# Kernel tuning notes

Hardware: AMD Instinct MI355X
Metric: run time of the kernel (lower is better)

## Reference

```python
import jax, jax.numpy as jnp
import numpy as np

HIDDEN = 2048
INTER = 768
N_EXPERTS = 16
TOP_K = 2
B, S = 4, 2048


def setup_inputs() -> dict:
    key = jax.random.key(0)
    ks = jax.random.split(key, 5)
    scale = 0.02
    return {
        "hidden_states": jax.random.normal(ks[0], (B, S, HIDDEN), dtype=jnp.float32),
        # nn.Linear weight layout: [out_features, in_features]
        "gate_w": jax.random.normal(ks[1], (N_EXPERTS, HIDDEN), dtype=jnp.float32) * scale,
        "w_gate": jax.random.normal(ks[2], (N_EXPERTS, INTER, HIDDEN), dtype=jnp.float32) * scale,
        "w_up": jax.random.normal(ks[3], (N_EXPERTS, INTER, HIDDEN), dtype=jnp.float32) * scale,
        "w_down": jax.random.normal(ks[4], (N_EXPERTS, HIDDEN, INTER), dtype=jnp.float32) * scale,
    }


def _moe_forward(hidden_states, gate_w, w_gate, w_up, w_down):
    b, s, h = hidden_states.shape
    x = hidden_states.reshape(-1, h)                      # [T, H]
    t = x.shape[0]
    logits = x @ gate_w.T                                 # [T, E]
    probs = jax.nn.softmax(logits, axis=-1)
    top_vals, top_idx = jax.lax.top_k(probs, TOP_K)       # [T, K]
    top_vals = top_vals / jnp.sum(top_vals, axis=-1, keepdims=True)
    # combine weights per token per expert (zero if not routed)
    comb = jnp.zeros((t, N_EXPERTS), dtype=x.dtype)
    comb = comb.at[jnp.arange(t)[:, None], top_idx].add(top_vals)  # [T, E]

    out = jnp.zeros_like(x)
    for e in range(N_EXPERTS):  # small fixed loop over experts
        g = x @ w_gate[e].T                               # [T, I]
        u = x @ w_up[e].T                                 # [T, I]
        y = (jax.nn.silu(g) * u) @ w_down[e].T            # [T, H]
        out = out + comb[:, e:e + 1] * y
    return out.reshape(b, s, h)


def reference(hidden_states, gate_w, w_gate, w_up, w_down):
    return _moe_forward(hidden_states, gate_w, w_gate, w_up, w_down)
```

## Files before the change

kernel.cpp:

```cpp
#include <hip/hip_runtime.h>
#include <hip/hip_bf16.h>

#define NTOK 8192
#define HID 2048
#define INTER 768
#define NEXP 16

typedef __bf16 bf16x8 __attribute__((ext_vector_type(8)));
typedef float f32x4 __attribute__((ext_vector_type(4)));

typedef const __attribute__((address_space(1))) void gvoid_t;
typedef __attribute__((address_space(3))) void lvoid_t;

static __device__ __forceinline__ void load_lds16(const void* g, void* l) {
  __builtin_amdgcn_global_load_lds((gvoid_t*)g, (lvoid_t*)l, 16, 0, 0);
}

static __device__ __forceinline__ unsigned short f2bf(float f) {
  unsigned int u = __float_as_uint(f);
  u += 0x7FFFu + ((u >> 16) & 1u);
  return (unsigned short)(u >> 16);
}

static __device__ __forceinline__ float bf2f(unsigned short b) {
  return __uint_as_float(((unsigned int)b) << 16);
}

#define SYNC_PIPE                                     \
  asm volatile("s_waitcnt vmcnt(0)" ::: "memory");    \
  __builtin_amdgcn_s_barrier();

__global__ __launch_bounds__(256) void cvt3_kernel(
    const float* __restrict__ s0, const float* __restrict__ s1, const float* __restrict__ s2,
    unsigned short* __restrict__ dst0, unsigned short* __restrict__ dst1,
    unsigned short* __restrict__ dst2, int n) {
  const float* src = (blockIdx.y == 0) ? s0 : (blockIdx.y == 1) ? s1 : s2;
  unsigned short* dst = (blockIdx.y == 0) ? dst0 : (blockIdx.y == 1) ? dst1 : dst2;
  int i = (blockIdx.x * 256 + threadIdx.x) * 4;
  int stride = gridDim.x * 256 * 4;
  for (; i < n; i += stride) {
    float4 v = *reinterpret_cast<const float4*>(src + i);
    ushort4 o;
    o.x = f2bf(v.x); o.y = f2bf(v.y); o.z = f2bf(v.z); o.w = f2bf(v.w);
    *reinterpret_cast<ushort4*>(dst + i) = o;
  }
}

__global__ __launch_bounds__(256) void router_kernel(const float* __restrict__ x,
                                                     const float* __restrict__ gw,
                                                     int* __restrict__ te,
                                                     float* __restrict__ tw,
                                                     unsigned short* __restrict__ Xb) {
  const int lane = threadIdx.x & 63;
  const int wid = threadIdx.x >> 6;
  const int t0 = (blockIdx.x * 4 + wid) * 2;
  const float4* xa = reinterpret_cast<const float4*>(x + (size_t)t0 * HID);
  const float4* xb = xa + HID / 4;
  const float4* g4 = reinterpret_cast<const float4*>(gw);

  float4 va[8], vb[8];
#pragma unroll
  for (int j = 0; j < 8; ++j) {
    va[j] = xa[lane + 64 * j];
    vb[j] = xb[lane + 64 * j];
  }
  ushort4* oa = reinterpret_cast<ushort4*>(Xb + (size_t)t0 * HID);
  ushort4* ob = oa + HID / 4;
#pragma unroll
  for (int j = 0; j < 8; ++j) {
    ushort4 u;
    u.x = f2bf(va[j].x); u.y = f2bf(va[j].y); u.z = f2bf(va[j].z); u.w = f2bf(va[j].w);
    oa[lane + 64 * j] = u;
    u.x = f2bf(vb[j].x); u.y = f2bf(vb[j].y); u.z = f2bf(vb[j].z); u.w = f2bf(vb[j].w);
    ob[lane + 64 * j] = u;
  }

  float accA[NEXP], accB[NEXP];
#pragma unroll
  for (int e = 0; e < NEXP; ++e) { accA[e] = 0.f; accB[e] = 0.f; }
#pragma unroll
  for (int e = 0; e < NEXP; ++e) {
#pragma unroll
    for (int j = 0; j < 8; ++j) {
      float4 g = g4[e * (HID / 4) + lane + 64 * j];
      accA[e] += va[j].x * g.x + va[j].y * g.y + va[j].z * g.z + va[j].w * g.w;
      accB[e] += vb[j].x * g.x + vb[j].y * g.y + vb[j].z * g.z + vb[j].w * g.w;
    }
  }
#pragma unroll
  for (int e = 0; e < NEXP; ++e) {
#pragma unroll
    for (int m = 32; m >= 1; m >>= 1) {
      accA[e] += __shfl_xor(accA[e], m);
      accB[e] += __shfl_xor(accB[e], m);
    }
  }
  if (lane == 0) {
#pragma unroll
    for (int k = 0; k < 2; ++k) {
      const float* acc = k ? accB : accA;
      int t = t0 + k;
      float b0 = -1e30f; int i0 = 0;
#pragma unroll
      for (int e = 0; e < NEXP; ++e) { if (acc[e] > b0) { b0 = acc[e]; i0 = e; } }
      float b1 = -1e30f; int i1 = 0;
#pragma unroll
      for (int e = 0; e < NEXP; ++e) { if (e != i0 && acc[e] > b1) { b1 = acc[e]; i1 = e; } }
      float w0 = 1.f / (1.f + __expf(b1 - b0));
      te[2 * t] = i0; te[2 * t + 1] = i1;
      tw[2 * t] = w0; tw[2 * t + 1] = 1.f - w0;
    }
  }
}

__global__ __launch_bounds__(256) void build_kernel(
    const int* __restrict__ te, const float* __restrict__ tw,
    int* __restrict__ counts, int* __restrict__ offsets,
    int* __restrict__ tok_flat, float* __restrict__ w_flat,
    int* __restrict__ tok_slot,
    int* __restrict__ tile_map, int* __restrict__ n_tiles) {
  __shared__ int lds_cnt[NEXP][257];
  __shared__ int lds_off[NEXP];
  const int tid = threadIdx.x;
  const int lane = tid & 63;
  const int wv = tid >> 6;

  int cnt[NEXP];
#pragma unroll
  for (int ex = 0; ex < NEXP; ++ex) cnt[ex] = 0;
  for (int i = 0; i < 64; ++i) {
    int e = te[tid * 64 + i];
#pragma unroll
    for (int ex = 0; ex < NEXP; ++ex) cnt[ex] += (e == ex) ? 1 : 0;
  }
#pragma unroll
  for (int ex = 0; ex < NEXP; ++ex) lds_cnt[ex][tid] = cnt[ex];
  __syncthreads();

  for (int ex = wv * 4; ex < wv * 4 + 4; ++ex) {
    int carry = 0;
    for (int c = 0; c < 4; ++c) {
      int v = lds_cnt[ex][c * 64 + lane];
      int s = v;
#pragma unroll
      for (int d = 1; d < 64; d <<= 1) {
        int o = __shfl_up(s, d);
        if (lane >= d) s += o;
      }
      lds_cnt[ex][c * 64 + lane] = carry + s - v;
      carry += __shfl(s, 63);
    }
    if (lane == 0) lds_cnt[ex][256] = carry;
  }
  __syncthreads();

  if (tid == 0) {
    int run = 0, nt = 0;
    for (int e = 0; e < NEXP; ++e) {
      int tot = lds_cnt[e][256];
      counts[e] = tot;
      offsets[e] = run;
      lds_off[e] = run;
      for (int m0 = 0; m0 < tot; m0 += 128) tile_map[nt++] = (e << 16) | m0;
      run += tot;
    }
    *n_tiles = nt;
  }
  __syncthreads();

  int base[NEXP];
#pragma unroll
  for (int ex = 0; ex < NEXP; ++ex) base[ex] = lds_off[ex] + lds_cnt[ex][tid];
  for (int i = 0; i < 64; ++i) {
    int idx = tid * 64 + i;
    int e = te[idx];
    float w = tw[idx];
    int pos = 0;
#pragma unroll
    for (int ex = 0; ex < NEXP; ++ex) {
      if (e == ex) { pos = base[ex]; base[ex] = pos + 1; }
    }
    tok_flat[pos] = idx >> 1;
    w_flat[pos] = w;
    tok_slot[idx] = pos;
  }
}

__global__ __launch_bounds__(256, 3) void gemm_gu_kernel(
    const unsigned short* __restrict__ Xb,
    const unsigned short* __restrict__ Wg,
    const unsigned short* __restrict__ Wu,
    const int* __restrict__ counts, const int* __restrict__ offsets,
    const int* __restrict__ tok_flat,
    const int* __restrict__ tile_map, const int* __restrict__ n_tiles,
    unsigned short* __restrict__ Hf) {
  const int bid = blockIdx.x;
  const int cpx = gridDim.x >> 3;
  const int wg = (bid & 7) * cpx + (bid >> 3);
  const int y = wg / 12;
  if (y >= *n_tiles) return;
  const int xb = wg - y * 12;
  const int tm = tile_map[y];
  const int e = tm >> 16, m0 = tm & 0xFFFF;
  const int cnt = counts[e];
  const int off = offsets[e];
  const int n0 = xb * 64;

  __shared__ __align__(16) unsigned short As0[128 * 32], As1[128 * 32];
  __shared__ __align__(16) unsigned short Bg0[64 * 32], Bg1[64 * 32];
  __shared__ __align__(16) unsigned short Bu0[64 * 32], Bu1[64 * 32];

  const int tid = threadIdx.x;
  const int lane = tid & 63;
  const int wid = tid >> 6;
  const int rl = tid >> 2;
  const int srcc = ((tid & 3) ^ ((tid >> 3) & 3)) * 8;
  const int d0 = tid * 8;
  const int d1 = d0 + 64 * 32;

  const int r0 = m0 + rl, r1 = r0 + 64;
  const int s0 = (r0 < cnt) ? off + r0 : off;
  const int s1 = (r1 < cnt) ? off + r1 : off;
  const unsigned short* aptr0 = Xb + (size_t)tok_flat[s0] * HID + srcc;
  const unsigned short* aptr1 = Xb + (size_t)tok_flat[s1] * HID + srcc;
  const unsigned short* gptr0 = Wg + ((size_t)e * INTER + n0 + rl) * HID + srcc;
  const unsigned short* uptr0 = Wu + ((size_t)e * INTER + n0 + rl) * HID + srcc;

  f32x4 zero = {0.f, 0.f, 0.f, 0.f};
  f32x4 accG[4][2], accU[4][2];
#pragma unroll
  for (int i = 0; i < 4; ++i)
#pragma unroll
    for (int j = 0; j < 2; ++j) { accG[i][j] = zero; accU[i][j] = zero; }

  const int wm = (wid >> 1) * 64;
  const int wn = (wid & 1) * 32;
  const int fr = lane & 15;
  const int cs = (((lane >> 4) ^ ((lane >> 1) & 3)) * 8);

#define STAGE_GU(AS, BGS, BUS, kt)           \
  {                                          \
    load_lds16(aptr0 + (kt), (AS) + d0);     \
    load_lds16(aptr1 + (kt), (AS) + d1);     \
    load_lds16(gptr0 + (kt), (BGS) + d0);    \
    load_lds16(uptr0 + (kt), (BUS) + d0);    \
  }

#define COMPUTE_GU(AS, BGS, BUS)                                                       \
  {                                                                                    \
    bf16x8 af[4], bg[2], bu[2];                                                        \
    _Pragma("unroll") for (int i = 0; i < 4; ++i)                                      \
      af[i] = *reinterpret_cast<const bf16x8*>((AS) + (wm + i * 16 + fr) * 32 + cs);   \
    _Pragma("unroll") for (int j = 0; j < 2; ++j) {                                    \
      bg[j] = *reinterpret_cast<const bf16x8*>((BGS) + (wn + j * 16 + fr) * 32 + cs);  \
      bu[j] = *reinterpret_cast<const bf16x8*>((BUS) + (wn + j * 16 + fr) * 32 + cs);  \
    }                                                                                  \
    _Pragma("unroll") for (int i = 0; i < 4; ++i)                                      \
      _Pragma("unroll") for (int j = 0; j < 2; ++j) {                                  \
        accG[i][j] = __builtin_amdgcn_mfma_f32_16x16x32_bf16(af[i], bg[j], accG[i][j], 0, 0, 0); \
        accU[i][j] = __builtin_amdgcn_mfma_f32_16x16x32_bf16(af[i], bu[j], accU[i][j], 0, 0, 0); \
      }                                                                                \
  }

  STAGE_GU(As0, Bg0, Bu0, 0);
  SYNC_PIPE
#pragma unroll 1
  for (int kt = 0; kt < HID; kt += 64) {
    STAGE_GU(As1, Bg1, Bu1, kt + 32);
    COMPUTE_GU(As0, Bg0, Bu0);
    SYNC_PIPE
    if (kt + 64 < HID) STAGE_GU(As0, Bg0, Bu0, kt + 64);
    COMPUTE_GU(As1, Bg1, Bu1);
    SYNC_PIPE
  }
#undef STAGE_GU
#undef COMPUTE_GU

  const int lr = (lane >> 4) * 4;
  const int lc = lane & 15;
#pragma unroll
  for (int i = 0; i < 4; ++i) {
#pragma unroll
    for (int r = 0; r < 4; ++r) {
      int m = wm + i * 16 + lr + r;
      if (m0 + m < cnt) {
        size_t base = (size_t)(off + m0 + m) * INTER + (size_t)(n0 + wn + lc);
#pragma unroll
        for (int j = 0; j < 2; ++j) {
          float g = accG[i][j][r];
          float u = accU[i][j][r];
          float h = g / (1.f + __expf(-g)) * u;
          Hf[base + j * 16] = f2bf(h);
        }
      }
    }
  }
}

__global__ __launch_bounds__(256, 4) void gemm_y_kernel(
    const unsigned short* __restrict__ Hf,
    const unsigned short* __restrict__ Wd,
    const int* __restrict__ counts, const int* __restrict__ offsets,
    const float* __restrict__ w_flat,
    const int* __restrict__ tile_map, const int* __restrict__ n_tiles,
    unsigned short* __restrict__ Yf) {
  const int bid = blockIdx.x;
  const int cpx = gridDim.x >> 3;
  const int wg = (bid & 7) * cpx + (bid >> 3);
  const int y = wg / 32;
  if (y >= *n_tiles) return;
  const int xb = wg - y * 32;
  const int tm = tile_map[y];
  const int e = tm >> 16, m0 = tm & 0xFFFF;
  const int cnt = counts[e];
  const int off = offsets[e];
  const int n0 = xb * 64;

  __shared__ __align__(16) unsigned short As0[128 * 32], As1[128 * 32];
  __shared__ __align__(16) unsigned short Bs0[64 * 32], Bs1[64 * 32];

  const int tid = threadIdx.x;
  const int lane = tid & 63;
  const int wid = tid >> 6;
  const int rl = tid >> 2;
  const int srcc = ((tid & 3) ^ ((tid >> 3) & 3)) * 8;
  const int d0 = tid * 8;
  const int d1 = d0 + 64 * 32;

  const int r0 = m0 + rl, r1 = r0 + 64;
  const int s0 = (r0 < cnt) ? off + r0 : off;
  const int s1 = (r1 < cnt) ? off + r1 : off;
  const unsigned short* aptr0 = Hf + (size_t)s0 * INTER + srcc;
  const unsigned short* aptr1 = Hf + (size_t)s1 * INTER + srcc;
  const unsigned short* bptr0 = Wd + ((size_t)e * HID + n0 + rl) * INTER + srcc;

  f32x4 zero = {0.f, 0.f, 0.f, 0.f};
  f32x4 acc[4][2];
#pragma unroll
  for (int i = 0; i < 4; ++i)
#pragma unroll
    for (int j = 0; j < 2; ++j) acc[i][j] = zero;

  const int wm = (wid >> 1) * 64;
  const int wn = (wid & 1) * 32;
  const int fr = lane & 15;
  const int cs = (((lane >> 4) ^ ((lane >> 1) & 3)) * 8);

#define STAGE_Y(AS, BS, kt)               \
  {                                       \
    load_lds16(aptr0 + (kt), (AS) + d0);  \
    load_lds16(aptr1 + (kt), (AS) + d1);  \
    load_lds16(bptr0 + (kt), (BS) + d0);  \
  }

#define COMPUTE_Y(AS, BS)                                                              \
  {                                                                                    \
    bf16x8 af[4], bf_[2];                                                              \
    _Pragma("unroll") for (int i = 0; i < 4; ++i)                                      \
      af[i] = *reinterpret_cast<const bf16x8*>((AS) + (wm + i * 16 + fr) * 32 + cs);   \
    _Pragma("unroll") for (int j = 0; j < 2; ++j)                                      \
      bf_[j] = *reinterpret_cast<const bf16x8*>((BS) + (wn + j * 16 + fr) * 32 + cs);  \
    _Pragma("unroll") for (int i = 0; i < 4; ++i)                                      \
      _Pragma("unroll") for (int j = 0; j < 2; ++j)                                    \
        acc[i][j] = __builtin_amdgcn_mfma_f32_16x16x32_bf16(af[i], bf_[j], acc[i][j], 0, 0, 0); \
  }

  STAGE_Y(As0, Bs0, 0);
  SYNC_PIPE
#pragma unroll 1
  for (int kt = 0; kt < INTER; kt += 64) {
    STAGE_Y(As1, Bs1, kt + 32);
    COMPUTE_Y(As0, Bs0);
    SYNC_PIPE
    if (kt + 64 < INTER) STAGE_Y(As0, Bs0, kt + 64);
    COMPUTE_Y(As1, Bs1);
    SYNC_PIPE
  }
#undef STAGE_Y
#undef COMPUTE_Y

  const int lr = (lane >> 4) * 4;
  const int lc = lane & 15;
#pragma unroll
  for (int i = 0; i < 4; ++i) {
#pragma unroll
    for (int r = 0; r < 4; ++r) {
      int m = wm + i * 16 + lr + r;
      if (m0 + m < cnt) {
        int slot = off + m0 + m;
        float w = w_flat[slot];
        size_t base = (size_t)slot * HID + (size_t)(n0 + wn + lc);
#pragma unroll
        for (int j = 0; j < 2; ++j) Yf[base + j * 16] = f2bf(w * acc[i][j][r]);
      }
    }
  }
}

__global__ __launch_bounds__(256) void combine_kernel(const unsigned short* __restrict__ Yf,
                                                      const int* __restrict__ tok_slot,
                                                      float* __restrict__ out) {
  const int t = blockIdx.x;
  const int c = threadIdx.x * 8;
  const int s0 = tok_slot[2 * t];
  const int s1 = tok_slot[2 * t + 1];
  const ushort4* p0 = reinterpret_cast<const ushort4*>(Yf + (size_t)s0 * HID + c);
  const ushort4* p1 = reinterpret_cast<const ushort4*>(Yf + (size_t)s1 * HID + c);
  ushort4 a0 = p0[0], a1 = p0[1];
  ushort4 b0 = p1[0], b1 = p1[1];
  float4 o0, o1;
  o0.x = bf2f(a0.x) + bf2f(b0.x);
  o0.y = bf2f(a0.y) + bf2f(b0.y);
  o0.z = bf2f(a0.z) + bf2f(b0.z);
  o0.w = bf2f(a0.w) + bf2f(b0.w);
  o1.x = bf2f(a1.x) + bf2f(b1.x);
  o1.y = bf2f(a1.y) + bf2f(b1.y);
  o1.z = bf2f(a1.z) + bf2f(b1.z);
  o1.w = bf2f(a1.w) + bf2f(b1.w);
  float4* op = reinterpret_cast<float4*>(out + (size_t)t * HID + c);
  op[0] = o0;
  op[1] = o1;
}

extern "C" void kernel_launch(void* const* d_in, const int* in_sizes, int n_in,
                              void* d_out, int out_size, void* d_ws, size_t ws_size,
                              hipStream_t stream) {
  const float* x  = (const float*)d_in[0];
  const float* gw = (const float*)d_in[1];
  const float* wg = (const float*)d_in[2];
  const float* wu = (const float*)d_in[3];
  const float* wd = (const float*)d_in[4];
  float* out = (float*)d_out;
  char* ws = (char*)d_ws;

  int*   counts   = (int*)(ws + 0);
  int*   offsets  = (int*)(ws + 128);
  int*   n_tiles  = (int*)(ws + 192);
  int*   tile_map = (int*)(ws + 256);
  int*   te       = (int*)(ws + 1024);
  float* tw       = (float*)(ws + 66560);
  int*   tok_flat = (int*)(ws + 132096);
  float* w_flat   = (float*)(ws + 197632);
  unsigned short* Xb  = (unsigned short*)(ws + 263168);
  unsigned short* Wgb = (unsigned short*)(ws + 33817600);
  unsigned short* Wub = (unsigned short*)(ws + 84149248);
  unsigned short* Wdb = (unsigned short*)(ws + 134480896);
  unsigned short* Hf  = (unsigned short*)(ws + 184812544);
  int*   tok_slot = (int*)(ws + 209978368);
  unsigned short* Yf  = Wgb;

  cvt3_kernel<<<dim3(1024, 3), 256, 0, stream>>>(wg, wu, wd, Wgb, Wub, Wdb,
                                                 NEXP * INTER * HID);
  router_kernel<<<NTOK / 8, 256, 0, stream>>>(x, gw, te, tw, Xb);
  build_kernel<<<1, 256, 0, stream>>>(te, tw, counts, offsets, tok_flat, w_flat,
                                      tok_slot, tile_map, n_tiles);

  gemm_gu_kernel<<<144 * 12, 256, 0, stream>>>(
      Xb, Wgb, Wub, counts, offsets, tok_flat, tile_map, n_tiles, Hf);
  gemm_y_kernel<<<144 * 32, 256, 0, stream>>>(
      Hf, Wdb, counts, offsets, w_flat, tile_map, n_tiles, Yf);
  combine_kernel<<<NTOK, 256, 0, stream>>>(Yf, tok_slot, out);
}
```

Baseline: 474.9 us.

## Triple-buffer LDS tiles with partial vmcnt waits in gate-up and down GEMMs

Both expert GEMM kernels move from double to triple buffering of the LDS tiles. Each phase now does one partial `s_waitcnt vmcnt` plus one barrier, then issues the load two chunks ahead and computes on the current chunk. This keeps a global load in flight during compute and halves the barrier count per K step. The cost is more LDS per block (about 48KB for gate-up), which may lower occupancy, and a hand-tuned vmcnt count that depends on the exact number of loads per stage.

```diff
diff --git a/kernel.cpp b/kernel.cpp
--- a/kernel.cpp
+++ b/kernel.cpp
@@ -26,9 +26,10 @@
   return __uint_as_float(((unsigned int)b) << 16);
 }
 
-#define SYNC_PIPE                                     \
-  asm volatile("s_waitcnt vmcnt(0)" ::: "memory");    \
-  __builtin_amdgcn_s_barrier();
+#define VMCNT_BAR(S)                                      \
+  asm volatile("s_waitcnt vmcnt(" S ")" ::: "memory");    \
+  __builtin_amdgcn_s_barrier();                           \
+  __builtin_amdgcn_sched_barrier(0);
 
 __global__ __launch_bounds__(256) void cvt3_kernel(
     const float* __restrict__ s0, const float* __restrict__ s1, const float* __restrict__ s2,
@@ -206,9 +207,9 @@
   const int off = offsets[e];
   const int n0 = xb * 64;
 
-  __shared__ __align__(16) unsigned short As0[128 * 32], As1[128 * 32];
-  __shared__ __align__(16) unsigned short Bg0[64 * 32], Bg1[64 * 32];
-  __shared__ __align__(16) unsigned short Bu0[64 * 32], Bu1[64 * 32];
+  __shared__ __align__(16) unsigned short As0[128 * 32], As1[128 * 32], As2[128 * 32];
+  __shared__ __align__(16) unsigned short Bg0[64 * 32], Bg1[64 * 32], Bg2[64 * 32];
+  __shared__ __align__(16) unsigned short Bu0[64 * 32], Bu1[64 * 32], Bu2[64 * 32];
 
   const int tid = threadIdx.x;
   const int lane = tid & 63;
@@ -262,17 +263,21 @@
       }                                                                                \
   }
 
+#define PHASE_GU(AS, BGS, BUS, NAS, NBGS, NBUS, nkt, S) \
+  VMCNT_BAR(S)                                          \
+  if ((nkt) < HID) STAGE_GU(NAS, NBGS, NBUS, (nkt));    \
+  COMPUTE_GU(AS, BGS, BUS)
+
   STAGE_GU(As0, Bg0, Bu0, 0);
-  SYNC_PIPE
+  STAGE_GU(As1, Bg1, Bu1, 32);
 #pragma unroll 1
-  for (int kt = 0; kt < HID; kt += 64) {
-    STAGE_GU(As1, Bg1, Bu1, kt + 32);
-    COMPUTE_GU(As0, Bg0, Bu0);
-    SYNC_PIPE
-    if (kt + 64 < HID) STAGE_GU(As0, Bg0, Bu0, kt + 64);
-    COMPUTE_GU(As1, Bg1, Bu1);
-    SYNC_PIPE
-  }
+  for (int p = 0; p < 63; p += 3) {
+    PHASE_GU(As0, Bg0, Bu0, As2, Bg2, Bu2, (p + 2) * 32, "4");
+    PHASE_GU(As1, Bg1, Bu1, As0, Bg0, Bu0, (p + 3) * 32, "4");
+    PHASE_GU(As2, Bg2, Bu2, As1, Bg1, Bu1, (p + 4) * 32, "4");
+  }
+  PHASE_GU(As0, Bg0, Bu0, As2, Bg2, Bu2, 65 * 32, "0");
+#undef PHASE_GU
 #undef STAGE_GU
 #undef COMPUTE_GU
 
@@ -316,8 +321,8 @@
   const int off = offsets[e];
   const int n0 = xb * 64;
 
-  __shared__ __align__(16) unsigned short As0[128 * 32], As1[128 * 32];
-  __shared__ __align__(16) unsigned short Bs0[64 * 32], Bs1[64 * 32];
+  __shared__ __align__(16) unsigned short As0[128 * 32], As1[128 * 32], As2[128 * 32];
+  __shared__ __align__(16) unsigned short Bs0[64 * 32], Bs1[64 * 32], Bs2[64 * 32];
 
   const int tid = threadIdx.x;
   const int lane = tid & 63;
@@ -365,17 +370,23 @@
         acc[i][j] = __builtin_amdgcn_mfma_f32_16x16x32_bf16(af[i], bf_[j], acc[i][j], 0, 0, 0); \
   }
 
+#define PHASE_Y(AS, BS, NAS, NBS, nkt, S)        \
+  VMCNT_BAR(S)                                   \
+  if ((nkt) < INTER) STAGE_Y(NAS, NBS, (nkt));   \
+  COMPUTE_Y(AS, BS)
+
   STAGE_Y(As0, Bs0, 0);
-  SYNC_PIPE
+  STAGE_Y(As1, Bs1, 32);
 #pragma unroll 1
-  for (int kt = 0; kt < INTER; kt += 64) {
-    STAGE_Y(As1, Bs1, kt + 32);
-    COMPUTE_Y(As0, Bs0);
-    SYNC_PIPE
-    if (kt + 64 < INTER) STAGE_Y(As0, Bs0, kt + 64);
-    COMPUTE_Y(As1, Bs1);
-    SYNC_PIPE
-  }
+  for (int p = 0; p < 21; p += 3) {
+    PHASE_Y(As0, Bs0, As2, Bs2, (p + 2) * 32, "3");
+    PHASE_Y(As1, Bs1, As0, Bs0, (p + 3) * 32, "3");
+    PHASE_Y(As2, Bs2, As1, Bs1, (p + 4) * 32, "3");
+  }
+  PHASE_Y(As0, Bs0, As2, Bs2, 23 * 32, "3");
+  PHASE_Y(As1, Bs1, As0, Bs0, 24 * 32, "3");
+  PHASE_Y(As2, Bs2, As1, Bs1, 25 * 32, "0");
+#undef PHASE_Y
 #undef STAGE_Y
 #undef COMPUTE_Y
 
```

Result: no change. 472.2 us (-0.6%).
